# Kernel optimization log

Hardware: AMD Instinct MI355X
Metric: run time of the kernel (lower is better)

The kernel has to match this reference:

```python
import jax, jax.numpy as jnp
import numpy as np
import math

T, B, I, H = 512, 64, 256, 512


def setup_inputs() -> dict:
    key = jax.random.key(0)
    ks = jax.random.split(key, 8)
    inp = {}
    inp["x"] = jax.random.normal(ks[0], (T, B, I), jnp.float32)
    # positive elapsed-time intervals per step/batch
    inp["time"] = jax.random.uniform(ks[1], (T, B), jnp.float32, 0.0, 2.0)
    def wn(k, shape, fan_in):
        return jax.random.normal(k, shape, jnp.float32) * (1.0 / math.sqrt(fan_in))
    # forward-direction cell params
    inp["W_ih_f"] = wn(ks[2], (I, 4 * H), I)
    inp["W_hh_f"] = wn(ks[3], (H, 4 * H), H)
    inp["b_f"] = jnp.zeros((4 * H,), jnp.float32)
    inp["W_d_f"] = wn(ks[4], (H, H), H)
    inp["b_d_f"] = jnp.zeros((H,), jnp.float32)
    # backward-direction cell params
    inp["W_ih_b"] = wn(ks[5], (I, 4 * H), I)
    inp["W_hh_b"] = wn(ks[6], (H, 4 * H), H)
    inp["b_b"] = jnp.zeros((4 * H,), jnp.float32)
    inp["W_d_b"] = wn(ks[7], (H, H), H)
    inp["b_d_b"] = jnp.zeros((H,), jnp.float32)
    return inp


def _run_direction(x, t, W_ih, W_hh, b, W_d, b_d):
    """Time-aware LSTM scan over leading axis. x: [T,B,I], t: [T,B]."""
    Bz = x.shape[1]
    Hh = W_hh.shape[0]
    E = jnp.float32(math.e)

    def step(carry, xt_tt):
        h, c = carry
        xt, tt = xt_tt  # [B,I], [B]
        # TLSTM-style time decay of short-term memory
        c_s = jnp.tanh(c @ W_d + b_d)                 # [B,H]
        c_s_hat = c_s / jnp.log(E + tt[:, None])      # decayed short-term
        c_adj = c - c_s + c_s_hat                     # adjusted cell memory
        gates = xt @ W_ih + h @ W_hh + b              # [B,4H]
        i, f, g, o = jnp.split(gates, 4, axis=-1)
        i = jax.nn.sigmoid(i)
        f = jax.nn.sigmoid(f)
        o = jax.nn.sigmoid(o)
        c_new = f * c_adj + i * jnp.tanh(g)
        h_new = o * jnp.tanh(c_new)
        return (h_new, c_new), h_new

    init = (jnp.zeros((Bz, Hh), x.dtype), jnp.zeros((Bz, Hh), x.dtype))
    _, ys = jax.lax.scan(step, init, (x, t))
    return ys  # [T,B,H]


def reference(x, time, W_ih_f, W_hh_f, b_f, W_d_f, b_d_f,
              W_ih_b, W_hh_b, b_b, W_d_b, b_d_b):
    out_f = _run_direction(x, time, W_ih_f, W_hh_f, b_f, W_d_f, b_d_f)
    # reverse direction: flip time axis, scan, flip outputs back
    out_b = _run_direction(x[::-1], time[::-1], W_ih_b, W_hh_b, b_b, W_d_b, b_d_b)[::-1]
    return jnp.concatenate([out_f, out_b], axis=-1)  # [T,B,2H]
```

## Files before the change

kernel.cpp:

```cpp
#include <hip/hip_runtime.h>
#include <cstdint>

#define T_DIM 512
#define B_DIM 64
#define I_DIM 256
#define H_DIM 512

typedef _Float16 f16x8 __attribute__((ext_vector_type(8)));
typedef float f32x4  __attribute__((ext_vector_type(4)));
typedef unsigned int u32x4 __attribute__((ext_vector_type(4)));

union H8U { f16x8 v; u32x4 u; };

#define WS_FLAGS   0u
#define WS_STATE   8192u
#define GRP_U32    16384u
#define WS_XPK     (8192u + 8u*65536u)
#define XPK_U32    (512u*4u*8u*64u*4u)
#define WS_NEED_MIN WS_XPK
#define WS_NEED_XPK (WS_XPK + XPK_U32*4u)

__device__ __forceinline__ unsigned short f2h(float f) {
  union { _Float16 h; unsigned short u; } c; c.h = (_Float16)f; return c.u;
}
__device__ __forceinline__ float sigm(float v) { return 1.0f / (1.0f + __expf(-v)); }
__device__ __forceinline__ float tanh_f(float v) {
  float e = __expf(2.0f * fabsf(v));
  float r = 1.0f - 2.0f / (e + 1.0f);
  return copysignf(r, v);
}

__device__ __forceinline__ void st_u32(unsigned* p, unsigned v) {
  asm volatile("global_store_dword %0, %1, off sc0 sc1" :: "v"(p), "v"(v) : "memory");
}
__device__ __forceinline__ unsigned ld_u32(const unsigned* p) {
  unsigned v;
  asm volatile("global_load_dword %0, %1, off sc0 sc1\n\ts_waitcnt vmcnt(0)"
               : "=v"(v) : "v"(p) : "memory");
  return v;
}

__global__ void __launch_bounds__(256) init_ws_kernel(unsigned* ws) {
  unsigned n = WS_STATE / 4u;
  for (unsigned i = blockIdx.x * 256u + threadIdx.x; i < n; i += gridDim.x * 256u)
    __hip_atomic_store(&ws[i], 0u, __ATOMIC_RELAXED, __HIP_MEMORY_SCOPE_AGENT);
}

__global__ void __launch_bounds__(256) xpack_kernel(const float* __restrict__ x,
                                                    unsigned* __restrict__ xpk) {
  size_t idx = (size_t)blockIdx.x * 256 + threadIdx.x;
  int l = (int)(idx & 63);
  size_t kt = (idx >> 6) & 7, mt = (idx >> 9) & 3, t = idx >> 11;
  const float* xp = x + ((t * 64) + mt * 16 + (size_t)(l & 15)) * 256 + kt * 32 + (size_t)(l >> 4) * 8;
  f32x4 a = *(const f32x4*)xp, b = *(const f32x4*)(xp + 4);
  float v[8] = {a[0], a[1], a[2], a[3], b[0], b[1], b[2], b[3]};
  u32x4 pk;
  #pragma unroll
  for (int i = 0; i < 4; ++i)
    pk[i] = (unsigned)f2h(v[2 * i]) | ((unsigned)f2h(v[2 * i + 1]) << 16);
  *(u32x4*)(xpk + idx * 4) = pk;
}

template <bool XPK>
__global__ void __launch_bounds__(256, 1) lstm_kernel(
    const float* __restrict__ x, const float* __restrict__ tim,
    const float* __restrict__ Wih_f, const float* __restrict__ Whh_f,
    const float* __restrict__ bias_f, const float* __restrict__ Wd_f,
    const float* __restrict__ bd_f,
    const float* __restrict__ Wih_b, const float* __restrict__ Whh_b,
    const float* __restrict__ bias_b, const float* __restrict__ Wd_b,
    const float* __restrict__ bd_b,
    float* __restrict__ out, char* __restrict__ wsb,
    const unsigned* __restrict__ xpk)
{
  const int tid = threadIdx.x;
  const int w   = tid >> 6;
  const int l   = tid & 63;
  const int lw  = l & 15;
  const int ko  = l >> 4;
  const int g   = blockIdx.x & 7;
  const int js  = blockIdx.x >> 3;
  const int dir = g & 1;
  const int mt  = g >> 1;
  const int b0  = mt * 16;

  const float* Wih  = dir ? Wih_b  : Wih_f;
  const float* Whh  = dir ? Whh_b  : Whh_f;
  const float* bias = dir ? bias_b : bias_f;
  const float* Wd   = dir ? Wd_b   : Wd_f;
  const float* bd   = dir ? bd_b   : bd_f;

  unsigned* flagbase = (unsigned*)(wsb + WS_FLAGS) + (size_t)g * 256;
  unsigned* state = (unsigned*)(wsb + WS_STATE) + (size_t)g * GRP_U32;

  __shared__ float red[4][5][16][34];

  f16x8 wx[4][2][2];
  f16x8 wh[4][4][2];
  f16x8 wd[4][2];
  #pragma unroll
  for (int xi = 0; xi < 2; ++xi) {
    const int krow = (w * 2 + xi) * 32 + ko * 8;
    #pragma unroll
    for (int g4 = 0; g4 < 4; ++g4) {
      #pragma unroll
      for (int ct = 0; ct < 2; ++ct) {
        const float* p = Wih + (size_t)krow * 2048 + g4 * 512 + js * 32 + ct * 16 + lw;
        #pragma unroll
        for (int i = 0; i < 8; ++i) wx[g4][xi][ct][i] = (_Float16)p[(size_t)i * 2048];
      }
    }
  }
  #pragma unroll
  for (int q = 0; q < 4; ++q) {
    const int krow = w * 128 + q * 32 + ko * 8;
    #pragma unroll
    for (int g4 = 0; g4 < 4; ++g4) {
      #pragma unroll
      for (int ct = 0; ct < 2; ++ct) {
        const float* p = Whh + (size_t)krow * 2048 + g4 * 512 + js * 32 + ct * 16 + lw;
        #pragma unroll
        for (int i = 0; i < 8; ++i) wh[g4][q][ct][i] = (_Float16)p[(size_t)i * 2048];
      }
    }
    #pragma unroll
    for (int ct = 0; ct < 2; ++ct) {
      const float* p2 = Wd + (size_t)krow * 512 + js * 32 + ct * 16 + lw;
      #pragma unroll
      for (int i = 0; i < 8; ++i) wd[q][ct][i] = (_Float16)p2[(size_t)i * 512];
    }
  }

  const int ub = tid >> 4;
  const int uj = tid & 15;
  float bs_i[2], bs_f[2], bs_g[2], bs_o[2], bs_d[2], c_reg[2];
  #pragma unroll
  for (int ct = 0; ct < 2; ++ct) {
    const int jg = js * 32 + ct * 16 + uj;
    bs_i[ct] = bias[jg];
    bs_f[ct] = bias[512 + jg];
    bs_g[ct] = bias[1024 + jg];
    bs_o[ct] = bias[1536 + jg];
    bs_d[ct] = bd[jg];
    c_reg[ct] = 0.0f;
  }

  u32x4 rr[4][2];
  u32x4 xpf0, xpf1;

#define ISSUE_KT(kt) do { \
    const unsigned* sp_ = state + (size_t)lslot * 8192 + (size_t)lw * 512 + w * 128 + (kt) * 32 + ko * 8; \
    asm volatile( \
        "global_load_dwordx4 %0, %2, off sc0 sc1\n\t" \
        "global_load_dwordx4 %1, %2, off offset:16 sc0 sc1" \
        : "=&v"(rr[kt][0]), "=&v"(rr[kt][1]) : "v"(sp_) : "memory"); \
  } while (0)

#define MFMA_KT(kt) do { \
    H8U hf_, cf_; \
    hf_.u[0] = __builtin_amdgcn_perm(rr[kt][0][1], rr[kt][0][0], 0x07060302u); \
    hf_.u[1] = __builtin_amdgcn_perm(rr[kt][0][3], rr[kt][0][2], 0x07060302u); \
    hf_.u[2] = __builtin_amdgcn_perm(rr[kt][1][1], rr[kt][1][0], 0x07060302u); \
    hf_.u[3] = __builtin_amdgcn_perm(rr[kt][1][3], rr[kt][1][2], 0x07060302u); \
    cf_.u[0] = __builtin_amdgcn_perm(rr[kt][0][1], rr[kt][0][0], 0x05040100u); \
    cf_.u[1] = __builtin_amdgcn_perm(rr[kt][0][3], rr[kt][0][2], 0x05040100u); \
    cf_.u[2] = __builtin_amdgcn_perm(rr[kt][1][1], rr[kt][1][0], 0x05040100u); \
    cf_.u[3] = __builtin_amdgcn_perm(rr[kt][1][3], rr[kt][1][2], 0x05040100u); \
    _Pragma("unroll") \
    for (int g4 = 0; g4 < 4; ++g4) { \
      _Pragma("unroll") \
      for (int ct = 0; ct < 2; ++ct) \
        ag[g4][ct] = __builtin_amdgcn_mfma_f32_16x16x32_f16(hf_.v, wh[g4][kt][ct], ag[g4][ct], 0, 0, 0); \
    } \
    _Pragma("unroll") \
    for (int ct = 0; ct < 2; ++ct) \
      ac[ct] = __builtin_amdgcn_mfma_f32_16x16x32_f16(cf_.v, wd[kt][ct], ac[ct], 0, 0, 0); \
  } while (0)

  if (XPK) {
    const int ts0 = dir ? (T_DIM - 1) : 0;
    const unsigned* xb = xpk + (((size_t)ts0 * 4 + mt) * 8 + w * 2) * 256 + (size_t)l * 4;
    asm volatile(
        "global_load_dwordx4 %0, %2, off\n\t"
        "global_load_dwordx4 %1, %3, off"
        : "=v"(xpf0), "=v"(xpf1) : "v"(xb), "v"(xb + 256) : "memory");
    asm volatile("s_waitcnt vmcnt(0)" ::: "memory");
    __builtin_amdgcn_sched_barrier(0);
  }

  for (int t = 0; t < T_DIM; ++t) {
    const int tsrc = dir ? (T_DIM - 1 - t) : t;
    const int sslot = t & 1;
    const int lslot = sslot ^ 1;

    float tt = tim[(size_t)tsrc * B_DIM + b0 + ub];

    f16x8 ax[2];
    if (XPK) {
      H8U u0, u1; u0.u = xpf0; u1.u = xpf1;
      ax[0] = u0.v; ax[1] = u1.v;
    } else {
      #pragma unroll
      for (int xi = 0; xi < 2; ++xi) {
        const float* xp = x + ((size_t)tsrc * B_DIM + b0 + lw) * I_DIM + (w * 2 + xi) * 32 + ko * 8;
        f32x4 v0 = *(const f32x4*)xp;
        f32x4 v1 = *(const f32x4*)(xp + 4);
        f16x8 vv;
        #pragma unroll
        for (int i = 0; i < 4; ++i) { vv[i] = (_Float16)v0[i]; vv[4 + i] = (_Float16)v1[i]; }
        ax[xi] = vv;
      }
    }

    f32x4 ag[4][2]; f32x4 ac[2];
    #pragma unroll
    for (int g4 = 0; g4 < 4; ++g4) { ag[g4][0] = (f32x4)0.0f; ag[g4][1] = (f32x4)0.0f; }
    ac[0] = (f32x4)0.0f; ac[1] = (f32x4)0.0f;

    #pragma unroll
    for (int xi = 0; xi < 2; ++xi) {
      #pragma unroll
      for (int g4 = 0; g4 < 4; ++g4) {
        #pragma unroll
        for (int ct = 0; ct < 2; ++ct)
          ag[g4][ct] = __builtin_amdgcn_mfma_f32_16x16x32_f16(ax[xi], wx[g4][xi][ct], ag[g4][ct], 0, 0, 0);
      }
    }

    if (t > 0) {
      if (l < 16) {
        const unsigned* fl = flagbase + (size_t)l * 16;
        while (ld_u32(fl) < (unsigned)t) { }
      }
      __builtin_amdgcn_sched_barrier(0);

      ISSUE_KT(0); ISSUE_KT(1); ISSUE_KT(2); ISSUE_KT(3);
      if (XPK) {
        const int tn = (t + 1 < T_DIM) ? (dir ? (T_DIM - 2 - t) : (t + 1)) : 0;
        const unsigned* xbn = xpk + (((size_t)tn * 4 + mt) * 8 + w * 2) * 256 + (size_t)l * 4;
        asm volatile(
            "global_load_dwordx4 %0, %2, off\n\t"
            "global_load_dwordx4 %1, %3, off"
            : "=v"(xpf0), "=v"(xpf1) : "v"(xbn), "v"(xbn + 256) : "memory");
      }

      if (XPK) { asm volatile("s_waitcnt vmcnt(8)" ::: "memory"); }
      else     { asm volatile("s_waitcnt vmcnt(6)" ::: "memory"); }
      __builtin_amdgcn_sched_barrier(0);
      MFMA_KT(0);
      if (XPK) { asm volatile("s_waitcnt vmcnt(6)" ::: "memory"); }
      else     { asm volatile("s_waitcnt vmcnt(4)" ::: "memory"); }
      __builtin_amdgcn_sched_barrier(0);
      MFMA_KT(1);
      if (XPK) { asm volatile("s_waitcnt vmcnt(4)" ::: "memory"); }
      else     { asm volatile("s_waitcnt vmcnt(2)" ::: "memory"); }
      __builtin_amdgcn_sched_barrier(0);
      MFMA_KT(2);
      if (XPK) { asm volatile("s_waitcnt vmcnt(2)" ::: "memory"); }
      else     { asm volatile("s_waitcnt vmcnt(0)" ::: "memory"); }
      __builtin_amdgcn_sched_barrier(0);
      MFMA_KT(3);
    } else if (XPK) {
      const int tn = dir ? (T_DIM - 2) : 1;
      const unsigned* xbn = xpk + (((size_t)tn * 4 + mt) * 8 + w * 2) * 256 + (size_t)l * 4;
      asm volatile(
          "global_load_dwordx4 %0, %2, off\n\t"
          "global_load_dwordx4 %1, %3, off"
          : "=v"(xpf0), "=v"(xpf1) : "v"(xbn), "v"(xbn + 256) : "memory");
    }

    #pragma unroll
    for (int g4 = 0; g4 < 4; ++g4) {
      #pragma unroll
      for (int ct = 0; ct < 2; ++ct) {
        f32x4 s = ag[g4][ct];
        #pragma unroll
        for (int r = 0; r < 4; ++r) red[w][g4][ko * 4 + r][ct * 16 + lw] = s[r];
      }
    }
    #pragma unroll
    for (int ct = 0; ct < 2; ++ct) {
      f32x4 s = ac[ct];
      #pragma unroll
      for (int r = 0; r < 4; ++r) red[w][4][ko * 4 + r][ct * 16 + lw] = s[r];
    }
    asm volatile("s_waitcnt lgkmcnt(0)" ::: "memory");
    __builtin_amdgcn_s_barrier();

    const float dinv = 1.0f / __logf(2.718281828459045f + tt);
    #pragma unroll
    for (int ct = 0; ct < 2; ++ct) {
      const int cj = ct * 16 + uj;
      float gi = red[0][0][ub][cj] + red[1][0][ub][cj] + red[2][0][ub][cj] + red[3][0][ub][cj] + bs_i[ct];
      float gf = red[0][1][ub][cj] + red[1][1][ub][cj] + red[2][1][ub][cj] + red[3][1][ub][cj] + bs_f[ct];
      float gg = red[0][2][ub][cj] + red[1][2][ub][cj] + red[2][2][ub][cj] + red[3][2][ub][cj] + bs_g[ct];
      float go = red[0][3][ub][cj] + red[1][3][ub][cj] + red[2][3][ub][cj] + red[3][3][ub][cj] + bs_o[ct];
      float csv = red[0][4][ub][cj] + red[1][4][ub][cj] + red[2][4][ub][cj] + red[3][4][ub][cj] + bs_d[ct];

      float c_s = tanh_f(csv);
      float c_adj = c_reg[ct] - c_s + c_s * dinv;
      float iv = sigm(gi);
      float fv = sigm(gf);
      float ov = sigm(go);
      float gv = tanh_f(gg);
      float c_new = fv * c_adj + iv * gv;
      float h_new = ov * tanh_f(c_new);
      c_reg[ct] = c_new;

      const int jglob = js * 32 + cj;
      unsigned val = ((unsigned)f2h(h_new) << 16) | (unsigned)f2h(c_new);
      unsigned* sp = state + (size_t)sslot * 8192 + (size_t)ub * 512 + jglob;
      st_u32(sp, val);
      out[((size_t)tsrc * B_DIM + b0 + ub) * 1024 + dir * 512 + jglob] = h_new;
    }

    asm volatile("s_waitcnt vmcnt(0)" ::: "memory");
    __syncthreads();
    if (tid == 0) st_u32(flagbase + (size_t)js * 16, (unsigned)(t + 1));
  }
#undef ISSUE_KT
#undef MFMA_KT
}

extern "C" void kernel_launch(void* const* d_in, const int* in_sizes, int n_in,
                              void* d_out, int out_size, void* d_ws, size_t ws_size,
                              hipStream_t stream) {
  (void)in_sizes; (void)n_in; (void)out_size;
  if (ws_size < (size_t)WS_NEED_MIN) return;
  const bool use_xpk = ws_size >= (size_t)WS_NEED_XPK;

  const float* x     = (const float*)d_in[0];
  const float* tim   = (const float*)d_in[1];
  const float* Wih_f = (const float*)d_in[2];
  const float* Whh_f = (const float*)d_in[3];
  const float* b_f   = (const float*)d_in[4];
  const float* Wd_f  = (const float*)d_in[5];
  const float* bd_f  = (const float*)d_in[6];
  const float* Wih_b = (const float*)d_in[7];
  const float* Whh_b = (const float*)d_in[8];
  const float* b_b   = (const float*)d_in[9];
  const float* Wd_b  = (const float*)d_in[10];
  const float* bd_b  = (const float*)d_in[11];
  float* out = (float*)d_out;
  char* ws = (char*)d_ws;
  unsigned* xpk = (unsigned*)(ws + WS_XPK);

  hipLaunchKernelGGL(init_ws_kernel, dim3(8), dim3(256), 0, stream, (unsigned*)ws);
  if (use_xpk) {
    hipLaunchKernelGGL(xpack_kernel, dim3(4096), dim3(256), 0, stream, x, xpk);
    hipLaunchKernelGGL((lstm_kernel<true>), dim3(128), dim3(256), 0, stream,
                       x, tim, Wih_f, Whh_f, b_f, Wd_f, bd_f,
                       Wih_b, Whh_b, b_b, Wd_b, bd_b, out, ws, xpk);
  } else {
    hipLaunchKernelGGL((lstm_kernel<false>), dim3(128), dim3(256), 0, stream,
                       x, tim, Wih_f, Whh_f, b_f, Wd_f, bd_f,
                       Wih_b, Whh_b, b_b, Wd_b, bd_b, out, ws, (const unsigned*)nullptr);
  }
}
```

Baseline: 1.714 ms.

## Tag state words with step parity to speculatively load before flag wait

Embeds a 3-bit step tag in the low mantissa bits of the packed fp16 cell value, so each consumer can check whether the state it loaded is current. State loads are issued before the flag spin, and stale chunks are reloaded until their tags match. The output store is moved after the flag release to take it off the critical path. In exchange the stored cell value loses three mantissa bits (it is re-centred before the MFMA), and the workspace init is widened to pre-fill the state area with a tag value that never matches.

```diff
diff --git a/kernel.cpp b/kernel.cpp
--- a/kernel.cpp
+++ b/kernel.cpp
@@ -41,9 +41,10 @@
 }
 
 __global__ void __launch_bounds__(256) init_ws_kernel(unsigned* ws) {
-  unsigned n = WS_STATE / 4u;
+  unsigned nf = WS_STATE / 4u;
+  unsigned n = WS_XPK / 4u;
   for (unsigned i = blockIdx.x * 256u + threadIdx.x; i < n; i += gridDim.x * 256u)
-    __hip_atomic_store(&ws[i], 0u, __ATOMIC_RELAXED, __HIP_MEMORY_SCOPE_AGENT);
+    __hip_atomic_store(&ws[i], (i < nf) ? 0u : 5u, __ATOMIC_RELAXED, __HIP_MEMORY_SCOPE_AGENT);
 }
 
 __global__ void __launch_bounds__(256) xpack_kernel(const float* __restrict__ x,
@@ -156,6 +157,12 @@
         : "=&v"(rr[kt][0]), "=&v"(rr[kt][1]) : "v"(sp_) : "memory"); \
   } while (0)
 
+#define TAGOK(kt) __all((int)( \
+    ((rr[kt][0][0] & 7u) == e3) & ((rr[kt][0][1] & 7u) == e3) & \
+    ((rr[kt][0][2] & 7u) == e3) & ((rr[kt][0][3] & 7u) == e3) & \
+    ((rr[kt][1][0] & 7u) == e3) & ((rr[kt][1][1] & 7u) == e3) & \
+    ((rr[kt][1][2] & 7u) == e3) & ((rr[kt][1][3] & 7u) == e3)))
+
 #define MFMA_KT(kt) do { \
     H8U hf_, cf_; \
     hf_.u[0] = __builtin_amdgcn_perm(rr[kt][0][1], rr[kt][0][0], 0x07060302u); \
@@ -167,6 +174,8 @@
     cf_.u[2] = __builtin_amdgcn_perm(rr[kt][1][1], rr[kt][1][0], 0x05040100u); \
     cf_.u[3] = __builtin_amdgcn_perm(rr[kt][1][3], rr[kt][1][2], 0x05040100u); \
     _Pragma("unroll") \
+    for (int j = 0; j < 4; ++j) cf_.u[j] = (cf_.u[j] & 0xFFF8FFF8u) | 0x00040004u; \
+    _Pragma("unroll") \
     for (int g4 = 0; g4 < 4; ++g4) { \
       _Pragma("unroll") \
       for (int ct = 0; ct < 2; ++ct) \
@@ -212,56 +221,9 @@
       }
     }
 
-    f32x4 ag[4][2]; f32x4 ac[2];
-    #pragma unroll
-    for (int g4 = 0; g4 < 4; ++g4) { ag[g4][0] = (f32x4)0.0f; ag[g4][1] = (f32x4)0.0f; }
-    ac[0] = (f32x4)0.0f; ac[1] = (f32x4)0.0f;
-
-    #pragma unroll
-    for (int xi = 0; xi < 2; ++xi) {
-      #pragma unroll
-      for (int g4 = 0; g4 < 4; ++g4) {
-        #pragma unroll
-        for (int ct = 0; ct < 2; ++ct)
-          ag[g4][ct] = __builtin_amdgcn_mfma_f32_16x16x32_f16(ax[xi], wx[g4][xi][ct], ag[g4][ct], 0, 0, 0);
-      }
-    }
-
-    if (t > 0) {
-      if (l < 16) {
-        const unsigned* fl = flagbase + (size_t)l * 16;
-        while (ld_u32(fl) < (unsigned)t) { }
-      }
-      __builtin_amdgcn_sched_barrier(0);
-
-      ISSUE_KT(0); ISSUE_KT(1); ISSUE_KT(2); ISSUE_KT(3);
-      if (XPK) {
-        const int tn = (t + 1 < T_DIM) ? (dir ? (T_DIM - 2 - t) : (t + 1)) : 0;
-        const unsigned* xbn = xpk + (((size_t)tn * 4 + mt) * 8 + w * 2) * 256 + (size_t)l * 4;
-        asm volatile(
-            "global_load_dwordx4 %0, %2, off\n\t"
-            "global_load_dwordx4 %1, %3, off"
-            : "=v"(xpf0), "=v"(xpf1) : "v"(xbn), "v"(xbn + 256) : "memory");
-      }
-
-      if (XPK) { asm volatile("s_waitcnt vmcnt(8)" ::: "memory"); }
-      else     { asm volatile("s_waitcnt vmcnt(6)" ::: "memory"); }
-      __builtin_amdgcn_sched_barrier(0);
-      MFMA_KT(0);
-      if (XPK) { asm volatile("s_waitcnt vmcnt(6)" ::: "memory"); }
-      else     { asm volatile("s_waitcnt vmcnt(4)" ::: "memory"); }
-      __builtin_amdgcn_sched_barrier(0);
-      MFMA_KT(1);
-      if (XPK) { asm volatile("s_waitcnt vmcnt(4)" ::: "memory"); }
-      else     { asm volatile("s_waitcnt vmcnt(2)" ::: "memory"); }
-      __builtin_amdgcn_sched_barrier(0);
-      MFMA_KT(2);
-      if (XPK) { asm volatile("s_waitcnt vmcnt(2)" ::: "memory"); }
-      else     { asm volatile("s_waitcnt vmcnt(0)" ::: "memory"); }
-      __builtin_amdgcn_sched_barrier(0);
-      MFMA_KT(3);
-    } else if (XPK) {
-      const int tn = dir ? (T_DIM - 2) : 1;
+    if (t > 0) { ISSUE_KT(0); ISSUE_KT(1); ISSUE_KT(2); ISSUE_KT(3); }
+    if (XPK) {
+      const int tn = (t + 1 < T_DIM) ? (dir ? (T_DIM - 2 - t) : (t + 1)) : 0;
       const unsigned* xbn = xpk + (((size_t)tn * 4 + mt) * 8 + w * 2) * 256 + (size_t)l * 4;
       asm volatile(
           "global_load_dwordx4 %0, %2, off\n\t"
@@ -269,6 +231,46 @@
           : "=v"(xpf0), "=v"(xpf1) : "v"(xbn), "v"(xbn + 256) : "memory");
     }
 
+    f32x4 ag[4][2]; f32x4 ac[2];
+    #pragma unroll
+    for (int g4 = 0; g4 < 4; ++g4) { ag[g4][0] = (f32x4)0.0f; ag[g4][1] = (f32x4)0.0f; }
+    ac[0] = (f32x4)0.0f; ac[1] = (f32x4)0.0f;
+    #pragma unroll
+    for (int xi = 0; xi < 2; ++xi) {
+      #pragma unroll
+      for (int g4 = 0; g4 < 4; ++g4) {
+        #pragma unroll
+        for (int ct = 0; ct < 2; ++ct)
+          ag[g4][ct] = __builtin_amdgcn_mfma_f32_16x16x32_f16(ax[xi], wx[g4][xi][ct], ag[g4][ct], 0, 0, 0);
+      }
+    }
+
+    if (t > 0) {
+      if (l < 16) {
+        const unsigned* fl = flagbase + (size_t)l * 16;
+        while (ld_u32(fl) < (unsigned)t) { }
+      }
+      asm volatile("s_waitcnt vmcnt(0)" ::: "memory");
+      __builtin_amdgcn_sched_barrier(0);
+
+      const unsigned e3 = (((unsigned)(t - 1)) >> 1) & 7u;
+      int f0 = !TAGOK(0), f1 = !TAGOK(1), f2 = !TAGOK(2), f3 = !TAGOK(3);
+      while (f0 | f1 | f2 | f3) {
+        if (f0) ISSUE_KT(0);
+        if (f1) ISSUE_KT(1);
+        if (f2) ISSUE_KT(2);
+        if (f3) ISSUE_KT(3);
+        asm volatile("s_waitcnt vmcnt(0)" ::: "memory");
+        __builtin_amdgcn_sched_barrier(0);
+        if (f0) f0 = !TAGOK(0);
+        if (f1) f1 = !TAGOK(1);
+        if (f2) f2 = !TAGOK(2);
+        if (f3) f3 = !TAGOK(3);
+      }
+
+      MFMA_KT(0); MFMA_KT(1); MFMA_KT(2); MFMA_KT(3);
+    }
+
     #pragma unroll
     for (int g4 = 0; g4 < 4; ++g4) {
       #pragma unroll
@@ -288,6 +290,8 @@
     __builtin_amdgcn_s_barrier();
 
     const float dinv = 1.0f / __logf(2.718281828459045f + tt);
+    const unsigned ptag = (((unsigned)t) >> 1) & 7u;
+    float h_keep[2];
     #pragma unroll
     for (int ct = 0; ct < 2; ++ct) {
       const int cj = ct * 16 + uj;
@@ -306,19 +310,23 @@
       float c_new = fv * c_adj + iv * gv;
       float h_new = ov * tanh_f(c_new);
       c_reg[ct] = c_new;
+      h_keep[ct] = h_new;
 
       const int jglob = js * 32 + cj;
-      unsigned val = ((unsigned)f2h(h_new) << 16) | (unsigned)f2h(c_new);
-      unsigned* sp = state + (size_t)sslot * 8192 + (size_t)ub * 512 + jglob;
-      st_u32(sp, val);
-      out[((size_t)tsrc * B_DIM + b0 + ub) * 1024 + dir * 512 + jglob] = h_new;
+      unsigned ch = ((unsigned)f2h(c_new) & 0xFFF8u) | ptag;
+      unsigned val = ((unsigned)f2h(h_new) << 16) | ch;
+      st_u32(state + (size_t)sslot * 8192 + (size_t)ub * 512 + jglob, val);
     }
 
     asm volatile("s_waitcnt vmcnt(0)" ::: "memory");
     __syncthreads();
     if (tid == 0) st_u32(flagbase + (size_t)js * 16, (unsigned)(t + 1));
+    #pragma unroll
+    for (int ct = 0; ct < 2; ++ct)
+      out[((size_t)tsrc * B_DIM + b0 + ub) * 1024 + dir * 512 + js * 32 + ct * 16 + uj] = h_keep[ct];
   }
 #undef ISSUE_KT
+#undef TAGOK
 #undef MFMA_KT
 }
 
@@ -345,7 +353,7 @@
   char* ws = (char*)d_ws;
   unsigned* xpk = (unsigned*)(ws + WS_XPK);
 
-  hipLaunchKernelGGL(init_ws_kernel, dim3(8), dim3(256), 0, stream, (unsigned*)ws);
+  hipLaunchKernelGGL(init_ws_kernel, dim3(64), dim3(256), 0, stream, (unsigned*)ws);
   if (use_xpk) {
     hipLaunchKernelGGL(xpack_kernel, dim3(4096), dim3(256), 0, stream, x, xpk);
     hipLaunchKernelGGL((lstm_kernel<true>), dim3(128), dim3(256), 0, stream,
```

New measurement: 1.895 ms. +10.6%, slower.
